# Kernel optimization log

Hardware: AMD Instinct MI355X
Metric: run time of the kernel (lower is better)

## Reference

```python
import jax, jax.numpy as jnp
import numpy as np

H = 1024
B = 8
T = 2048

def setup_inputs() -> dict:
    key = jax.random.key(0)
    ks = jax.random.split(key, 12)
    s = 1.0 / np.sqrt(H)
    return {
        "x": jax.random.normal(ks[0], (B, T, H), dtype=jnp.float32),
        "time_decay": jax.random.normal(ks[1], (H,), dtype=jnp.float32) * 0.1,
        "time_first": jax.random.normal(ks[2], (H,), dtype=jnp.float32) * 0.1,
        "time_mix_key": jax.random.uniform(ks[3], (1, 1, H), dtype=jnp.float32),
        "time_mix_value": jax.random.uniform(ks[4], (1, 1, H), dtype=jnp.float32),
        "time_mix_receptance": jax.random.uniform(ks[5], (1, 1, H), dtype=jnp.float32),
        "Wk": jax.random.normal(ks[6], (H, H), dtype=jnp.float32) * s,
        "Wv": jax.random.normal(ks[7], (H, H), dtype=jnp.float32) * s,
        "Wr": jax.random.normal(ks[8], (H, H), dtype=jnp.float32) * s,
        "Wo": jax.random.normal(ks[9], (H, H), dtype=jnp.float32) * s,
        "bo": jax.random.normal(ks[10], (H,), dtype=jnp.float32) * 0.01,
    }

def reference(x, time_decay, time_first, time_mix_key, time_mix_value,
              time_mix_receptance, Wk, Wv, Wr, Wo, bo):
    # time shift: shifted[:, t] = x[:, t-1], shifted[:, 0] = 0
    shifted = jnp.pad(x, ((0, 0), (1, 0), (0, 0)))[:, :-1]
    k_in = x * time_mix_key + shifted * (1.0 - time_mix_key)
    v_in = x * time_mix_value + shifted * (1.0 - time_mix_value)
    r_in = x * time_mix_receptance + shifted * (1.0 - time_mix_receptance)
    k = jnp.einsum('bth,oh->bto', k_in, Wk)
    v = jnp.einsum('bth,oh->bto', v_in, Wv)
    r = jax.nn.sigmoid(jnp.einsum('bth,oh->bto', r_in, Wr))

    td = jnp.exp(-jnp.exp(time_decay))  # (H,)

    def step(carry, kv):
        num, den = carry            # (B, H) each
        k_t, v_t = kv               # (B, H) each
        e = jnp.exp(time_first + k_t)
        out_t = (num + e * v_t) / (den + e)
        ek = jnp.exp(k_t)
        return (td * num + ek * v_t, td * den + ek), out_t

    init = (jnp.zeros((x.shape[0], x.shape[2]), x.dtype),
            jnp.zeros((x.shape[0], x.shape[2]), x.dtype))
    # scan over time: (T, B, H)
    _, wkv = jax.lax.scan(step, init, (k.transpose(1, 0, 2), v.transpose(1, 0, 2)))
    wkv = wkv.transpose(1, 0, 2)    # (B, T, H)

    return jnp.einsum('bth,oh->bto', r * wkv, Wo) + bo
```

## Files before the change

kernel.cpp:

```cpp
#include <hip/hip_runtime.h>
#include <hip/hip_bf16.h>
#include <cstdint>
#include <cstddef>

#define HH 1024
#define BB 8
#define TT 2048
#define MM (BB*TT)
#define CC 128
#define LL (TT/CC)

typedef __attribute__((ext_vector_type(8))) short bf16x8;
typedef __attribute__((ext_vector_type(8))) unsigned short u16x8;
typedef __attribute__((ext_vector_type(4))) float f32x4;

__device__ __forceinline__ unsigned short f2bf(float f) {
  union { float f; unsigned u; } v; v.f = f;
  return (unsigned short)((v.u + 0x7fffu + ((v.u >> 16) & 1u)) >> 16);
}
__device__ __forceinline__ float bf2f(unsigned short s) {
  union { float f; unsigned u; } v; v.u = ((unsigned)s) << 16;
  return v.f;
}

__device__ __forceinline__ void load_lds16(const void* g, void* l) {
  __builtin_amdgcn_global_load_lds((const __attribute__((address_space(1))) void*)g,
                                   (__attribute__((address_space(3))) void*)l,
                                   16, 0, 0);
}

__global__ __launch_bounds__(256) void conv_w(const float* __restrict__ Wk,
    const float* __restrict__ Wv, const float* __restrict__ Wr,
    const float* __restrict__ Wo, unsigned short* __restrict__ dst) {
  const int i = (blockIdx.x * 256 + threadIdx.x) * 4;
  const float* src = blockIdx.y == 0 ? Wk : blockIdx.y == 1 ? Wv : blockIdx.y == 2 ? Wr : Wo;
  const float4 v = *(const float4*)(src + i);
  ushort4 o; o.x = f2bf(v.x); o.y = f2bf(v.y); o.z = f2bf(v.z); o.w = f2bf(v.w);
  *(ushort4*)(dst + (size_t)blockIdx.y * HH * HH + i) = o;
}

__global__ __launch_bounds__(256) void mix_kernel(const float* __restrict__ x,
    const float* __restrict__ tmk, const float* __restrict__ tmv, const float* __restrict__ tmr,
    unsigned short* __restrict__ kin, unsigned short* __restrict__ vin,
    unsigned short* __restrict__ rin) {
  const int gid = blockIdx.x * 256 + threadIdx.x;
  const size_t e0 = (size_t)gid * 4;
  const int h = (int)(e0 & (HH - 1));
  const int t = (int)((e0 >> 10) & (TT - 1));
  const float4 xv = *(const float4*)(x + e0);
  float4 sv = make_float4(0.f, 0.f, 0.f, 0.f);
  if (t != 0) sv = *(const float4*)(x + e0 - HH);
  const float4 k4 = *(const float4*)(tmk + h);
  const float4 v4 = *(const float4*)(tmv + h);
  const float4 r4 = *(const float4*)(tmr + h);
  ushort4 ko, vo, ro;
  ko.x = f2bf(sv.x + k4.x * (xv.x - sv.x)); ko.y = f2bf(sv.y + k4.y * (xv.y - sv.y));
  ko.z = f2bf(sv.z + k4.z * (xv.z - sv.z)); ko.w = f2bf(sv.w + k4.w * (xv.w - sv.w));
  vo.x = f2bf(sv.x + v4.x * (xv.x - sv.x)); vo.y = f2bf(sv.y + v4.y * (xv.y - sv.y));
  vo.z = f2bf(sv.z + v4.z * (xv.z - sv.z)); vo.w = f2bf(sv.w + v4.w * (xv.w - sv.w));
  ro.x = f2bf(sv.x + r4.x * (xv.x - sv.x)); ro.y = f2bf(sv.y + r4.y * (xv.y - sv.y));
  ro.z = f2bf(sv.z + r4.z * (xv.z - sv.z)); ro.w = f2bf(sv.w + r4.w * (xv.w - sv.w));
  *(ushort4*)(kin + e0) = ko;
  *(ushort4*)(vin + e0) = vo;
  *(ushort4*)(rin + e0) = ro;
}


#define BAR()   do { asm volatile("" ::: "memory"); __builtin_amdgcn_s_barrier(); \
                     asm volatile("" ::: "memory"); } while (0)
#define LGKM0() asm volatile("s_waitcnt lgkmcnt(0)" ::: "memory")
#define VM6()   asm volatile("s_waitcnt vmcnt(6)" ::: "memory")
#define VM0()   asm volatile("s_waitcnt vmcnt(0)" ::: "memory")

__device__ __forceinline__ void stA(const unsigned short* __restrict__ Ag, int m0, int kt,
                                    unsigned short* buf, int h, int w, int rl, int scol) {
#pragma unroll
  for (int l = 0; l < 2; ++l) {
    const int row = l * 128 + h * 64 + w * 8;
    load_lds16(Ag + (size_t)(m0 + row + rl) * HH + kt + scol, buf + row * 64);
  }
}
__device__ __forceinline__ void stB(const unsigned short* __restrict__ Bg, int n0, int kt,
                                    unsigned short* buf, int h, int w, int rl, int scol) {
#pragma unroll
  for (int l = 0; l < 2; ++l) {
    const int row = (2 * (l * 2 + (w >> 2)) + h) * 32 + (w & 3) * 8;
    load_lds16(Bg + (size_t)(n0 + row + rl) * HH + kt + scol, buf + row * 64);
  }
}

template<int MH>
__device__ __forceinline__ void rdA(const unsigned short* buf, bf16x8 (&af)[4][2],
                                    int wm, int l15, int kq, int swz) {
#pragma unroll
  for (int fm = 0; fm < 4; ++fm)
#pragma unroll
    for (int kk = 0; kk < 2; ++kk)
      af[fm][kk] = *(const bf16x8*)(buf + (wm * 128 + MH * 64 + fm * 16 + l15) * 64
                                        + ((kk * 32 + kq * 8) ^ swz));
}
template<int NH>
__device__ __forceinline__ void rdB(const unsigned short* buf, bf16x8 (&bfr)[2][2][2],
                                    int wn, int l15, int kq, int swz) {
#pragma unroll
  for (int fn = 0; fn < 2; ++fn)
#pragma unroll
    for (int kk = 0; kk < 2; ++kk)
      bfr[NH][fn][kk] = *(const bf16x8*)(buf + (wn * 64 + NH * 32 + fn * 16 + l15) * 64
                                             + ((kk * 32 + kq * 8) ^ swz));
}
template<int MH, int NH>
__device__ __forceinline__ void mfmaQ(f32x4 (&acc)[8][4], const bf16x8 (&af)[4][2],
                                      const bf16x8 (&bfr)[2][2][2]) {
  __builtin_amdgcn_s_setprio(1);
#pragma unroll
  for (int kk = 0; kk < 2; ++kk)
#pragma unroll
    for (int fm = 0; fm < 4; ++fm)
#pragma unroll
      for (int fn = 0; fn < 2; ++fn)
        acc[MH * 4 + fm][NH * 2 + fn] = __builtin_amdgcn_mfma_f32_16x16x32_bf16(
            af[fm][kk], bfr[NH][fn][kk], acc[MH * 4 + fm][NH * 2 + fn], 0, 0, 0);
  __builtin_amdgcn_s_setprio(0);
}

__device__ __forceinline__ void gemm256(const unsigned short* __restrict__ Ag,
                                        const unsigned short* __restrict__ Bg,
                                        const int m0, const int n0,
                                        unsigned short* As, unsigned short* Bs,
                                        f32x4 (&acc)[8][4]) {
  const int tid = threadIdx.x;
  const int lane = tid & 63;
  const int w = tid >> 6;
  const int wm = w >> 2, wn = w & 3;
  const int l15 = lane & 15, kq = lane >> 4;
  const int swz = (l15 & 7) << 3;
  const int rl = lane >> 3;
  const int scol = ((lane & 7) ^ rl) * 8;
  unsigned short* const A0 = As;
  unsigned short* const A1 = As + 256 * 64;
  unsigned short* const B0 = Bs;
  unsigned short* const B1 = Bs + 256 * 64;
  bf16x8 af[4][2], bfr[2][2][2];

  stA(Ag, m0, 0, A0, 0, w, rl, scol);
  stB(Bg, n0, 0, B0, 0, w, rl, scol);
  stB(Bg, n0, 0, B0, 1, w, rl, scol);
  stA(Ag, m0, 0, A0, 1, w, rl, scol);
  stA(Ag, m0, 64, A1, 0, w, rl, scol);
  stB(Bg, n0, 64, B1, 0, w, rl, scol);
  stB(Bg, n0, 64, B1, 1, w, rl, scol);
  VM6(); BAR();

#pragma unroll 1
  for (int i = 0; i < 8; ++i) {
    const int tb1 = ((2 * i + 1) * 64) & (HH - 1);
    const int tn0 = ((2 * i + 2) * 64) & (HH - 1);
    const int tn1 = ((2 * i + 3) * 64) & (HH - 1);
    rdA<0>(A0, af, wm, l15, kq, swz); rdB<0>(B0, bfr, wn, l15, kq, swz);
    stA(Ag, m0, tb1, A1, 1, w, rl, scol);
    BAR(); LGKM0(); mfmaQ<0, 0>(acc, af, bfr); BAR();
    rdB<1>(B0, bfr, wn, l15, kq, swz);
    stA(Ag, m0, tn0, A0, 0, w, rl, scol);
    BAR(); LGKM0(); mfmaQ<0, 1>(acc, af, bfr); BAR();
    rdA<1>(A0, af, wm, l15, kq, swz);
    stB(Bg, n0, tn0, B0, 0, w, rl, scol);
    BAR(); LGKM0(); mfmaQ<1, 1>(acc, af, bfr); BAR();
    stB(Bg, n0, tn0, B0, 1, w, rl, scol);
    VM6(); BAR(); LGKM0(); mfmaQ<1, 0>(acc, af, bfr); BAR();
    rdA<0>(A1, af, wm, l15, kq, swz); rdB<0>(B1, bfr, wn, l15, kq, swz);
    stA(Ag, m0, tn0, A0, 1, w, rl, scol);
    BAR(); LGKM0(); mfmaQ<0, 0>(acc, af, bfr); BAR();
    rdB<1>(B1, bfr, wn, l15, kq, swz);
    stA(Ag, m0, tn1, A1, 0, w, rl, scol);
    BAR(); LGKM0(); mfmaQ<0, 1>(acc, af, bfr); BAR();
    rdA<1>(A1, af, wm, l15, kq, swz);
    stB(Bg, n0, tn1, B1, 0, w, rl, scol);
    BAR(); LGKM0(); mfmaQ<1, 1>(acc, af, bfr); BAR();
    stB(Bg, n0, tn1, B1, 1, w, rl, scol);
    VM6(); BAR(); LGKM0(); mfmaQ<1, 0>(acc, af, bfr); BAR();
  }
  VM0();
}

__device__ __forceinline__ void swizzle_mn256(int x, int& m0, int& n0) {
  const int wg = (x & 7) * 32 + (x >> 3);
  m0 = (wg >> 2) * 256;
  n0 = (wg & 3) * 256;
}

__global__ __launch_bounds__(512, 2) void gemm_kvr(const unsigned short* __restrict__ kin,
    const unsigned short* __restrict__ vin, const unsigned short* __restrict__ rin,
    const unsigned short* __restrict__ Wbf,
    unsigned short* __restrict__ kb, unsigned short* __restrict__ vb,
    unsigned short* __restrict__ rb) {
  __shared__ unsigned short As[2 * 256 * 64];
  __shared__ unsigned short Bs[2 * 256 * 64];
  const int z = blockIdx.y;
  const unsigned short* Ag = z == 0 ? kin : (z == 1 ? vin : rin);
  const unsigned short* Bg = Wbf + (size_t)z * HH * HH;
  unsigned short* Cg = z == 0 ? kb : (z == 1 ? vb : rb);
  int m0, n0; swizzle_mn256(blockIdx.x, m0, n0);
  f32x4 acc[8][4] = {};
  gemm256(Ag, Bg, m0, n0, As, Bs, acc);
  const int lane = threadIdx.x & 63, w = threadIdx.x >> 6;
  const int wm = w >> 2, wn = w & 3, l15 = lane & 15, lq = lane >> 4;
  const bool sig = (z == 2);
#pragma unroll
  for (int fm = 0; fm < 8; ++fm)
#pragma unroll
    for (int fn = 0; fn < 4; ++fn) {
      const int col = n0 + wn * 64 + fn * 16 + l15;
      const int r0 = m0 + wm * 128 + fm * 16 + lq * 4;
#pragma unroll
      for (int j = 0; j < 4; ++j) {
        float vv = acc[fm][fn][j];
        if (sig) vv = 1.0f / (1.0f + __expf(-vv));
        Cg[(size_t)(r0 + j) * HH + col] = f2bf(vv);
      }
    }
}

__global__ __launch_bounds__(512, 2) void gemm_o(const unsigned short* __restrict__ Ag,
    const unsigned short* __restrict__ Bg, const float* __restrict__ bias,
    float* __restrict__ C) {
  __shared__ unsigned short As[2 * 256 * 64];
  __shared__ unsigned short Bs[2 * 256 * 64];
  int m0, n0; swizzle_mn256(blockIdx.x, m0, n0);
  f32x4 acc[8][4] = {};
  gemm256(Ag, Bg, m0, n0, As, Bs, acc);
  const int lane = threadIdx.x & 63, w = threadIdx.x >> 6;
  const int wm = w >> 2, wn = w & 3, l15 = lane & 15, lq = lane >> 4;
#pragma unroll
  for (int fm = 0; fm < 8; ++fm)
#pragma unroll
    for (int fn = 0; fn < 4; ++fn) {
      const int col = n0 + wn * 64 + fn * 16 + l15;
      const float bv = bias[col];
      const int r0 = m0 + wm * 128 + fm * 16 + lq * 4;
#pragma unroll
      for (int j = 0; j < 4; ++j)
        C[(size_t)(r0 + j) * HH + col] = acc[fm][fn][j] + bv;
    }
}

__global__ __launch_bounds__(256) void wkv_part(const unsigned short* __restrict__ k,
    const unsigned short* __restrict__ v, const float* __restrict__ tdec,
    float* __restrict__ pnum, float* __restrict__ pden) {
  const int gid = blockIdx.x * 256 + threadIdx.x;
  const int h0 = (gid & 127) * 8;
  const int b = (gid >> 7) & (BB - 1);
  const int c = gid >> 10;
  float td[8], num[8], den[8];
#pragma unroll
  for (int j = 0; j < 8; ++j) {
    td[j] = __expf(-__expf(tdec[h0 + j]));
    num[j] = 0.f; den[j] = 0.f;
  }
  size_t idx = (size_t)b * TT * HH + (size_t)(c * LL) * HH + h0;
#pragma unroll 4
  for (int i = 0; i < LL; ++i, idx += HH) {
    const u16x8 k8 = *(const u16x8*)(k + idx);
    const u16x8 v8 = *(const u16x8*)(v + idx);
#pragma unroll
    for (int j = 0; j < 8; ++j) {
      const float ek = __expf(bf2f(k8[j]));
      num[j] = td[j] * num[j] + ek * bf2f(v8[j]);
      den[j] = td[j] * den[j] + ek;
    }
  }
  const size_t o = (size_t)c * (BB * HH) + b * HH + h0;
#pragma unroll
  for (int j = 0; j < 8; ++j) { pnum[o + j] = num[j]; pden[o + j] = den[j]; }
}

__global__ __launch_bounds__(256) void wkv_scan(const float* __restrict__ tdec,
    float* __restrict__ pnum, float* __restrict__ pden) {
  const int bh = blockIdx.x * 256 + threadIdx.x;
  const int h = bh & (HH - 1);
  const float ed = __expf(tdec[h]);
  const float tdL = __expf(-ed * (float)LL);
  float num = 0.f, den = 0.f;
#pragma unroll 8
  for (int c = 0; c < CC; ++c) {
    const size_t o = (size_t)c * (BB * HH) + bh;
    const float tn = pnum[o], td_ = pden[o];
    pnum[o] = num; pden[o] = den;
    num = tdL * num + tn;
    den = tdL * den + td_;
  }
}

__global__ __launch_bounds__(256) void wkv_final(const unsigned short* __restrict__ k,
    const unsigned short* __restrict__ v, const unsigned short* __restrict__ r,
    const float* __restrict__ tdec, const float* __restrict__ tfst,
    const float* __restrict__ pnum, const float* __restrict__ pden,
    unsigned short* __restrict__ rwkv) {
  const int gid = blockIdx.x * 256 + threadIdx.x;
  const int h0 = (gid & 127) * 8;
  const int b = (gid >> 7) & (BB - 1);
  const int c = gid >> 10;
  float td[8], etf[8], num[8], den[8];
  const size_t o = (size_t)c * (BB * HH) + b * HH + h0;
#pragma unroll
  for (int j = 0; j < 8; ++j) {
    td[j] = __expf(-__expf(tdec[h0 + j]));
    etf[j] = __expf(tfst[h0 + j]);
    num[j] = pnum[o + j]; den[j] = pden[o + j];
  }
  size_t idx = (size_t)b * TT * HH + (size_t)(c * LL) * HH + h0;
#pragma unroll 2
  for (int i = 0; i < LL; ++i, idx += HH) {
    const u16x8 k8 = *(const u16x8*)(k + idx);
    const u16x8 v8 = *(const u16x8*)(v + idx);
    const u16x8 r8 = *(const u16x8*)(r + idx);
    u16x8 o8;
#pragma unroll
    for (int j = 0; j < 8; ++j) {
      const float ek = __expf(bf2f(k8[j]));
      const float vt = bf2f(v8[j]);
      const float rt = bf2f(r8[j]);
      const float e = ek * etf[j];
      const float inv = __builtin_amdgcn_rcpf(den[j] + e);
      const float outv = (num[j] + e * vt) * inv;
      num[j] = td[j] * num[j] + ek * vt;
      den[j] = td[j] * den[j] + ek;
      o8[j] = f2bf(outv * rt);
    }
    *(u16x8*)(rwkv + idx) = o8;
  }
}

extern "C" void kernel_launch(void* const* d_in, const int* in_sizes, int n_in,
                              void* d_out, int out_size, void* d_ws, size_t ws_size,
                              hipStream_t stream) {
  (void)in_sizes; (void)n_in; (void)out_size; (void)ws_size;
  const float* x    = (const float*)d_in[0];
  const float* tdec = (const float*)d_in[1];
  const float* tfst = (const float*)d_in[2];
  const float* tmk  = (const float*)d_in[3];
  const float* tmv  = (const float*)d_in[4];
  const float* tmr  = (const float*)d_in[5];
  const float* Wk   = (const float*)d_in[6];
  const float* Wv   = (const float*)d_in[7];
  const float* Wr   = (const float*)d_in[8];
  const float* Wo   = (const float*)d_in[9];
  const float* bo   = (const float*)d_in[10];
  float* out = (float*)d_out;

  char* ws = (char*)d_ws;
  const size_t MiB = (size_t)1 << 20;
  unsigned short* Wbf = (unsigned short*)(ws);
  unsigned short* kin = (unsigned short*)(ws + 8 * MiB);
  unsigned short* vin = (unsigned short*)(ws + 40 * MiB);
  unsigned short* rin = (unsigned short*)(ws + 72 * MiB);
  unsigned short* rb  = (unsigned short*)(ws + 104 * MiB);
  unsigned short* kb = (unsigned short*)out;
  unsigned short* vb = kb + (size_t)MM * HH;
  unsigned short* rwkv = kin;
  float* pnum = (float*)(ws + 40 * MiB);
  float* pden = (float*)(ws + 44 * MiB);

  hipLaunchKernelGGL(conv_w, dim3(1024, 4), dim3(256), 0, stream, Wk, Wv, Wr, Wo, Wbf);
  hipLaunchKernelGGL(mix_kernel, dim3(16384), dim3(256), 0, stream,
                     x, tmk, tmv, tmr, kin, vin, rin);
  hipLaunchKernelGGL(gemm_kvr, dim3(256, 3), dim3(512), 0, stream,
                     kin, vin, rin, Wbf, kb, vb, rb);
  hipLaunchKernelGGL(wkv_part, dim3(512), dim3(256), 0, stream,
                     kb, vb, tdec, pnum, pden);
  hipLaunchKernelGGL(wkv_scan, dim3(32), dim3(256), 0, stream,
                     tdec, pnum, pden);
  hipLaunchKernelGGL(wkv_final, dim3(512), dim3(256), 0, stream,
                     kb, vb, rb, tdec, tfst, pnum, pden, rwkv);
  hipLaunchKernelGGL(gemm_o, dim3(256), dim3(512), 0, stream,
                     rwkv, Wbf + (size_t)3 * HH * HH, bo, out);
}
```

Measured before the change: 348.0 us.

## Reschedule GEMM main loop, transpose MFMA outputs for vector stores, double scan chunks

Restructures the bf16 GEMM inner loop: LDS fragment reads are split into halves with sched_barriers, the MFMA operands are swapped so each lane holds four consecutive columns, and the prefetch order changes so the loop waits at vmcnt(4) instead of vmcnt(6). Epilogues in both GEMMs now write ushort4/float4 vector stores instead of scalar strided stores. The WKV chunk count doubles to 256 with fully unrolled shorter chunks and twice the grid, and the pden buffer offset moves to fit. The intent is to overlap LDS reads, global prefetch and MFMAs better, coalesce output writes, and expose more parallelism in the scan, at the cost of more partial-state traffic and register pressure.

```diff
diff --git a/kernel.cpp b/kernel.cpp
--- a/kernel.cpp
+++ b/kernel.cpp
@@ -7,7 +7,7 @@
 #define BB 8
 #define TT 2048
 #define MM (BB*TT)
-#define CC 128
+#define CC 256
 #define LL (TT/CC)
 
 typedef __attribute__((ext_vector_type(8))) short bf16x8;
@@ -68,8 +68,8 @@
 
 #define BAR()   do { asm volatile("" ::: "memory"); __builtin_amdgcn_s_barrier(); \
                      asm volatile("" ::: "memory"); } while (0)
-#define LGKM0() asm volatile("s_waitcnt lgkmcnt(0)" ::: "memory")
-#define VM6()   asm volatile("s_waitcnt vmcnt(6)" ::: "memory")
+#define SB0()   __builtin_amdgcn_sched_barrier(0)
+#define VM4()   asm volatile("s_waitcnt vmcnt(4)" ::: "memory")
 #define VM0()   asm volatile("s_waitcnt vmcnt(0)" ::: "memory")
 
 __device__ __forceinline__ void stA(const unsigned short* __restrict__ Ag, int m0, int kt,
@@ -89,11 +89,11 @@
   }
 }
 
-template<int MH>
-__device__ __forceinline__ void rdA(const unsigned short* buf, bf16x8 (&af)[4][2],
-                                    int wm, int l15, int kq, int swz) {
-#pragma unroll
-  for (int fm = 0; fm < 4; ++fm)
+template<int MH, int FH>
+__device__ __forceinline__ void rdA_h(const unsigned short* buf, bf16x8 (&af)[4][2],
+                                      int wm, int l15, int kq, int swz) {
+#pragma unroll
+  for (int fm = FH * 2; fm < FH * 2 + 2; ++fm)
 #pragma unroll
     for (int kk = 0; kk < 2; ++kk)
       af[fm][kk] = *(const bf16x8*)(buf + (wm * 128 + MH * 64 + fm * 16 + l15) * 64
@@ -109,19 +109,17 @@
       bfr[NH][fn][kk] = *(const bf16x8*)(buf + (wn * 64 + NH * 32 + fn * 16 + l15) * 64
                                              + ((kk * 32 + kq * 8) ^ swz));
 }
-template<int MH, int NH>
-__device__ __forceinline__ void mfmaQ(f32x4 (&acc)[8][4], const bf16x8 (&af)[4][2],
+template<int MH, int NH, int FH>
+__device__ __forceinline__ void mfma8(f32x4 (&acc)[8][4], const bf16x8 (&af)[4][2],
                                       const bf16x8 (&bfr)[2][2][2]) {
-  __builtin_amdgcn_s_setprio(1);
 #pragma unroll
   for (int kk = 0; kk < 2; ++kk)
 #pragma unroll
-    for (int fm = 0; fm < 4; ++fm)
+    for (int fm = FH * 2; fm < FH * 2 + 2; ++fm)
 #pragma unroll
       for (int fn = 0; fn < 2; ++fn)
         acc[MH * 4 + fm][NH * 2 + fn] = __builtin_amdgcn_mfma_f32_16x16x32_bf16(
-            af[fm][kk], bfr[NH][fn][kk], acc[MH * 4 + fm][NH * 2 + fn], 0, 0, 0);
-  __builtin_amdgcn_s_setprio(0);
+            bfr[NH][fn][kk], af[fm][kk], acc[MH * 4 + fm][NH * 2 + fn], 0, 0, 0);
 }
 
 __device__ __forceinline__ void gemm256(const unsigned short* __restrict__ Ag,
@@ -149,36 +147,69 @@
   stA(Ag, m0, 0, A0, 1, w, rl, scol);
   stA(Ag, m0, 64, A1, 0, w, rl, scol);
   stB(Bg, n0, 64, B1, 0, w, rl, scol);
-  stB(Bg, n0, 64, B1, 1, w, rl, scol);
-  VM6(); BAR();
+  VM4();
+  BAR();
 
 #pragma unroll 1
   for (int i = 0; i < 8; ++i) {
-    const int tb1 = ((2 * i + 1) * 64) & (HH - 1);
+    const int t1  = ((2 * i + 1) * 64) & (HH - 1);
     const int tn0 = ((2 * i + 2) * 64) & (HH - 1);
     const int tn1 = ((2 * i + 3) * 64) & (HH - 1);
-    rdA<0>(A0, af, wm, l15, kq, swz); rdB<0>(B0, bfr, wn, l15, kq, swz);
-    stA(Ag, m0, tb1, A1, 1, w, rl, scol);
-    BAR(); LGKM0(); mfmaQ<0, 0>(acc, af, bfr); BAR();
+
+    rdA_h<0, 0>(A0, af, wm, l15, kq, swz); SB0();
+    rdB<0>(B0, bfr, wn, l15, kq, swz);     SB0();
+    rdA_h<0, 1>(A0, af, wm, l15, kq, swz); SB0();
     rdB<1>(B0, bfr, wn, l15, kq, swz);
+    stB(Bg, n0, t1, B1, 1, w, rl, scol);
+    stA(Ag, m0, t1, A1, 1, w, rl, scol);
+    BAR(); SB0();
+    __builtin_amdgcn_s_setprio(1);
+    mfma8<0, 0, 0>(acc, af, bfr); SB0();
+    mfma8<0, 0, 1>(acc, af, bfr); SB0();
+    mfma8<0, 1, 0>(acc, af, bfr);
+    mfma8<0, 1, 1>(acc, af, bfr);
+    __builtin_amdgcn_s_setprio(0);
+    BAR();
+    rdA_h<1, 0>(A0, af, wm, l15, kq, swz); SB0();
+    rdA_h<1, 1>(A0, af, wm, l15, kq, swz);
     stA(Ag, m0, tn0, A0, 0, w, rl, scol);
-    BAR(); LGKM0(); mfmaQ<0, 1>(acc, af, bfr); BAR();
-    rdA<1>(A0, af, wm, l15, kq, swz);
     stB(Bg, n0, tn0, B0, 0, w, rl, scol);
-    BAR(); LGKM0(); mfmaQ<1, 1>(acc, af, bfr); BAR();
+    BAR(); SB0();
+    __builtin_amdgcn_s_setprio(1);
+    mfma8<1, 0, 0>(acc, af, bfr);
+    mfma8<1, 1, 0>(acc, af, bfr); SB0();
+    mfma8<1, 0, 1>(acc, af, bfr);
+    mfma8<1, 1, 1>(acc, af, bfr);
+    __builtin_amdgcn_s_setprio(0);
+    VM4();
+    BAR();
+    rdA_h<0, 0>(A1, af, wm, l15, kq, swz); SB0();
+    rdB<0>(B1, bfr, wn, l15, kq, swz);     SB0();
+    rdA_h<0, 1>(A1, af, wm, l15, kq, swz); SB0();
+    rdB<1>(B1, bfr, wn, l15, kq, swz);
     stB(Bg, n0, tn0, B0, 1, w, rl, scol);
-    VM6(); BAR(); LGKM0(); mfmaQ<1, 0>(acc, af, bfr); BAR();
-    rdA<0>(A1, af, wm, l15, kq, swz); rdB<0>(B1, bfr, wn, l15, kq, swz);
     stA(Ag, m0, tn0, A0, 1, w, rl, scol);
-    BAR(); LGKM0(); mfmaQ<0, 0>(acc, af, bfr); BAR();
-    rdB<1>(B1, bfr, wn, l15, kq, swz);
+    BAR(); SB0();
+    __builtin_amdgcn_s_setprio(1);
+    mfma8<0, 0, 0>(acc, af, bfr); SB0();
+    mfma8<0, 0, 1>(acc, af, bfr); SB0();
+    mfma8<0, 1, 0>(acc, af, bfr);
+    mfma8<0, 1, 1>(acc, af, bfr);
+    __builtin_amdgcn_s_setprio(0);
+    BAR();
+    rdA_h<1, 0>(A1, af, wm, l15, kq, swz); SB0();
+    rdA_h<1, 1>(A1, af, wm, l15, kq, swz);
     stA(Ag, m0, tn1, A1, 0, w, rl, scol);
-    BAR(); LGKM0(); mfmaQ<0, 1>(acc, af, bfr); BAR();
-    rdA<1>(A1, af, wm, l15, kq, swz);
     stB(Bg, n0, tn1, B1, 0, w, rl, scol);
-    BAR(); LGKM0(); mfmaQ<1, 1>(acc, af, bfr); BAR();
-    stB(Bg, n0, tn1, B1, 1, w, rl, scol);
-    VM6(); BAR(); LGKM0(); mfmaQ<1, 0>(acc, af, bfr); BAR();
+    BAR(); SB0();
+    __builtin_amdgcn_s_setprio(1);
+    mfma8<1, 0, 0>(acc, af, bfr);
+    mfma8<1, 1, 0>(acc, af, bfr); SB0();
+    mfma8<1, 0, 1>(acc, af, bfr);
+    mfma8<1, 1, 1>(acc, af, bfr);
+    __builtin_amdgcn_s_setprio(0);
+    VM4();
+    BAR();
   }
   VM0();
 }
@@ -207,18 +238,21 @@
   const int wm = w >> 2, wn = w & 3, l15 = lane & 15, lq = lane >> 4;
   const bool sig = (z == 2);
 #pragma unroll
-  for (int fm = 0; fm < 8; ++fm)
+  for (int fm = 0; fm < 8; ++fm) {
+    const size_t mrow = (size_t)(m0 + wm * 128 + fm * 16 + l15) * HH;
 #pragma unroll
     for (int fn = 0; fn < 4; ++fn) {
-      const int col = n0 + wn * 64 + fn * 16 + l15;
-      const int r0 = m0 + wm * 128 + fm * 16 + lq * 4;
-#pragma unroll
-      for (int j = 0; j < 4; ++j) {
-        float vv = acc[fm][fn][j];
-        if (sig) vv = 1.0f / (1.0f + __expf(-vv));
-        Cg[(size_t)(r0 + j) * HH + col] = f2bf(vv);
+      const int ncol = n0 + wn * 64 + fn * 16 + lq * 4;
+      float v0 = acc[fm][fn][0], v1 = acc[fm][fn][1];
+      float v2 = acc[fm][fn][2], v3 = acc[fm][fn][3];
+      if (sig) {
+        v0 = 1.0f / (1.0f + __expf(-v0)); v1 = 1.0f / (1.0f + __expf(-v1));
+        v2 = 1.0f / (1.0f + __expf(-v2)); v3 = 1.0f / (1.0f + __expf(-v3));
       }
+      ushort4 o; o.x = f2bf(v0); o.y = f2bf(v1); o.z = f2bf(v2); o.w = f2bf(v3);
+      *(ushort4*)(Cg + mrow + ncol) = o;
     }
+  }
 }
 
 __global__ __launch_bounds__(512, 2) void gemm_o(const unsigned short* __restrict__ Ag,
@@ -232,16 +266,18 @@
   const int lane = threadIdx.x & 63, w = threadIdx.x >> 6;
   const int wm = w >> 2, wn = w & 3, l15 = lane & 15, lq = lane >> 4;
 #pragma unroll
-  for (int fm = 0; fm < 8; ++fm)
+  for (int fm = 0; fm < 8; ++fm) {
+    const size_t mrow = (size_t)(m0 + wm * 128 + fm * 16 + l15) * HH;
 #pragma unroll
     for (int fn = 0; fn < 4; ++fn) {
-      const int col = n0 + wn * 64 + fn * 16 + l15;
-      const float bv = bias[col];
-      const int r0 = m0 + wm * 128 + fm * 16 + lq * 4;
-#pragma unroll
-      for (int j = 0; j < 4; ++j)
-        C[(size_t)(r0 + j) * HH + col] = acc[fm][fn][j] + bv;
+      const int ncol = n0 + wn * 64 + fn * 16 + lq * 4;
+      const float4 bv = *(const float4*)(bias + ncol);
+      float4 ov;
+      ov.x = acc[fm][fn][0] + bv.x; ov.y = acc[fm][fn][1] + bv.y;
+      ov.z = acc[fm][fn][2] + bv.z; ov.w = acc[fm][fn][3] + bv.w;
+      *(float4*)(C + mrow + ncol) = ov;
     }
+  }
 }
 
 __global__ __launch_bounds__(256) void wkv_part(const unsigned short* __restrict__ k,
@@ -258,7 +294,7 @@
     num[j] = 0.f; den[j] = 0.f;
   }
   size_t idx = (size_t)b * TT * HH + (size_t)(c * LL) * HH + h0;
-#pragma unroll 4
+#pragma unroll
   for (int i = 0; i < LL; ++i, idx += HH) {
     const u16x8 k8 = *(const u16x8*)(k + idx);
     const u16x8 v8 = *(const u16x8*)(v + idx);
@@ -309,7 +345,7 @@
     num[j] = pnum[o + j]; den[j] = pden[o + j];
   }
   size_t idx = (size_t)b * TT * HH + (size_t)(c * LL) * HH + h0;
-#pragma unroll 2
+#pragma unroll
   for (int i = 0; i < LL; ++i, idx += HH) {
     const u16x8 k8 = *(const u16x8*)(k + idx);
     const u16x8 v8 = *(const u16x8*)(v + idx);
@@ -359,18 +395,18 @@
   unsigned short* vb = kb + (size_t)MM * HH;
   unsigned short* rwkv = kin;
   float* pnum = (float*)(ws + 40 * MiB);
-  float* pden = (float*)(ws + 44 * MiB);
+  float* pden = (float*)(ws + 48 * MiB);
 
   hipLaunchKernelGGL(conv_w, dim3(1024, 4), dim3(256), 0, stream, Wk, Wv, Wr, Wo, Wbf);
   hipLaunchKernelGGL(mix_kernel, dim3(16384), dim3(256), 0, stream,
                      x, tmk, tmv, tmr, kin, vin, rin);
   hipLaunchKernelGGL(gemm_kvr, dim3(256, 3), dim3(512), 0, stream,
                      kin, vin, rin, Wbf, kb, vb, rb);
-  hipLaunchKernelGGL(wkv_part, dim3(512), dim3(256), 0, stream,
+  hipLaunchKernelGGL(wkv_part, dim3(1024), dim3(256), 0, stream,
                      kb, vb, tdec, pnum, pden);
   hipLaunchKernelGGL(wkv_scan, dim3(32), dim3(256), 0, stream,
                      tdec, pnum, pden);
-  hipLaunchKernelGGL(wkv_final, dim3(512), dim3(256), 0, stream,
+  hipLaunchKernelGGL(wkv_final, dim3(1024), dim3(256), 0, stream,
                      kb, vb, rb, tdec, tfst, pnum, pden, rwkv);
   hipLaunchKernelGGL(gemm_o, dim3(256), dim3(512), 0, stream,
                      rwkv, Wbf + (size_t)3 * HH * HH, bo, out);
```

Result: slower. 374.1 us (+7.5%).

## Fuse prep kernels, swap MFMA operands for vectorized epilogue stores, adjust waits

Applied to the files above, without the earlier changes.

Merges the weight conversion and token-mix kernels into one launch to save a kernel launch. Swaps the A/B operands of the MFMA so each lane holds four consecutive columns, which lets the GEMM epilogues write ushort4/float4 vectors instead of scattered scalar stores. Drops the explicit lgkmcnt(0) waits and leaves LDS wait insertion to the compiler, moves setprio to wrap each MFMA group, and reorders the LDS reads.

```diff
diff --git a/kernel.cpp b/kernel.cpp
--- a/kernel.cpp
+++ b/kernel.cpp
@@ -29,48 +29,52 @@
                                    16, 0, 0);
 }
 
-__global__ __launch_bounds__(256) void conv_w(const float* __restrict__ Wk,
-    const float* __restrict__ Wv, const float* __restrict__ Wr,
-    const float* __restrict__ Wo, unsigned short* __restrict__ dst) {
-  const int i = (blockIdx.x * 256 + threadIdx.x) * 4;
-  const float* src = blockIdx.y == 0 ? Wk : blockIdx.y == 1 ? Wv : blockIdx.y == 2 ? Wr : Wo;
-  const float4 v = *(const float4*)(src + i);
-  ushort4 o; o.x = f2bf(v.x); o.y = f2bf(v.y); o.z = f2bf(v.z); o.w = f2bf(v.w);
-  *(ushort4*)(dst + (size_t)blockIdx.y * HH * HH + i) = o;
-}
-
-__global__ __launch_bounds__(256) void mix_kernel(const float* __restrict__ x,
+__global__ __launch_bounds__(256) void prep(const float* __restrict__ x,
     const float* __restrict__ tmk, const float* __restrict__ tmv, const float* __restrict__ tmr,
+    const float* __restrict__ Wk, const float* __restrict__ Wv,
+    const float* __restrict__ Wr, const float* __restrict__ Wo,
     unsigned short* __restrict__ kin, unsigned short* __restrict__ vin,
-    unsigned short* __restrict__ rin) {
-  const int gid = blockIdx.x * 256 + threadIdx.x;
-  const size_t e0 = (size_t)gid * 4;
-  const int h = (int)(e0 & (HH - 1));
-  const int t = (int)((e0 >> 10) & (TT - 1));
-  const float4 xv = *(const float4*)(x + e0);
-  float4 sv = make_float4(0.f, 0.f, 0.f, 0.f);
-  if (t != 0) sv = *(const float4*)(x + e0 - HH);
-  const float4 k4 = *(const float4*)(tmk + h);
-  const float4 v4 = *(const float4*)(tmv + h);
-  const float4 r4 = *(const float4*)(tmr + h);
-  ushort4 ko, vo, ro;
-  ko.x = f2bf(sv.x + k4.x * (xv.x - sv.x)); ko.y = f2bf(sv.y + k4.y * (xv.y - sv.y));
-  ko.z = f2bf(sv.z + k4.z * (xv.z - sv.z)); ko.w = f2bf(sv.w + k4.w * (xv.w - sv.w));
-  vo.x = f2bf(sv.x + v4.x * (xv.x - sv.x)); vo.y = f2bf(sv.y + v4.y * (xv.y - sv.y));
-  vo.z = f2bf(sv.z + v4.z * (xv.z - sv.z)); vo.w = f2bf(sv.w + v4.w * (xv.w - sv.w));
-  ro.x = f2bf(sv.x + r4.x * (xv.x - sv.x)); ro.y = f2bf(sv.y + r4.y * (xv.y - sv.y));
-  ro.z = f2bf(sv.z + r4.z * (xv.z - sv.z)); ro.w = f2bf(sv.w + r4.w * (xv.w - sv.w));
-  *(ushort4*)(kin + e0) = ko;
-  *(ushort4*)(vin + e0) = vo;
-  *(ushort4*)(rin + e0) = ro;
+    unsigned short* __restrict__ rin, unsigned short* __restrict__ Wbf) {
+  const int bx = blockIdx.x;
+  if (bx < 16384) {
+    const int gid = bx * 256 + threadIdx.x;
+    const size_t e0 = (size_t)gid * 4;
+    const int h = (int)(e0 & (HH - 1));
+    const int t = (int)((e0 >> 10) & (TT - 1));
+    const float4 xv = *(const float4*)(x + e0);
+    float4 sv = make_float4(0.f, 0.f, 0.f, 0.f);
+    if (t != 0) sv = *(const float4*)(x + e0 - HH);
+    const float4 k4 = *(const float4*)(tmk + h);
+    const float4 v4 = *(const float4*)(tmv + h);
+    const float4 r4 = *(const float4*)(tmr + h);
+    ushort4 ko, vo, ro;
+    ko.x = f2bf(sv.x + k4.x * (xv.x - sv.x)); ko.y = f2bf(sv.y + k4.y * (xv.y - sv.y));
+    ko.z = f2bf(sv.z + k4.z * (xv.z - sv.z)); ko.w = f2bf(sv.w + k4.w * (xv.w - sv.w));
+    vo.x = f2bf(sv.x + v4.x * (xv.x - sv.x)); vo.y = f2bf(sv.y + v4.y * (xv.y - sv.y));
+    vo.z = f2bf(sv.z + v4.z * (xv.z - sv.z)); vo.w = f2bf(sv.w + v4.w * (xv.w - sv.w));
+    ro.x = f2bf(sv.x + r4.x * (xv.x - sv.x)); ro.y = f2bf(sv.y + r4.y * (xv.y - sv.y));
+    ro.z = f2bf(sv.z + r4.z * (xv.z - sv.z)); ro.w = f2bf(sv.w + r4.w * (xv.w - sv.w));
+    *(ushort4*)(kin + e0) = ko;
+    *(ushort4*)(vin + e0) = vo;
+    *(ushort4*)(rin + e0) = ro;
+  } else {
+    const int q = bx - 16384;
+    const int zz = q >> 10;
+    const float* src = zz == 0 ? Wk : zz == 1 ? Wv : zz == 2 ? Wr : Wo;
+    const int i = ((q & 1023) * 256 + threadIdx.x) * 4;
+    const float4 v = *(const float4*)(src + i);
+    ushort4 o; o.x = f2bf(v.x); o.y = f2bf(v.y); o.z = f2bf(v.z); o.w = f2bf(v.w);
+    *(ushort4*)(Wbf + (size_t)zz * HH * HH + i) = o;
+  }
 }
 
 
 #define BAR()   do { asm volatile("" ::: "memory"); __builtin_amdgcn_s_barrier(); \
                      asm volatile("" ::: "memory"); } while (0)
-#define LGKM0() asm volatile("s_waitcnt lgkmcnt(0)" ::: "memory")
 #define VM6()   asm volatile("s_waitcnt vmcnt(6)" ::: "memory")
 #define VM0()   asm volatile("s_waitcnt vmcnt(0)" ::: "memory")
+#define PRIO1() __builtin_amdgcn_s_setprio(1)
+#define PRIO0() __builtin_amdgcn_s_setprio(0)
 
 __device__ __forceinline__ void stA(const unsigned short* __restrict__ Ag, int m0, int kt,
                                     unsigned short* buf, int h, int w, int rl, int scol) {
@@ -93,9 +97,9 @@
 __device__ __forceinline__ void rdA(const unsigned short* buf, bf16x8 (&af)[4][2],
                                     int wm, int l15, int kq, int swz) {
 #pragma unroll
-  for (int fm = 0; fm < 4; ++fm)
-#pragma unroll
-    for (int kk = 0; kk < 2; ++kk)
+  for (int kk = 0; kk < 2; ++kk)
+#pragma unroll
+    for (int fm = 0; fm < 4; ++fm)
       af[fm][kk] = *(const bf16x8*)(buf + (wm * 128 + MH * 64 + fm * 16 + l15) * 64
                                         + ((kk * 32 + kq * 8) ^ swz));
 }
@@ -103,16 +107,15 @@
 __device__ __forceinline__ void rdB(const unsigned short* buf, bf16x8 (&bfr)[2][2][2],
                                     int wn, int l15, int kq, int swz) {
 #pragma unroll
-  for (int fn = 0; fn < 2; ++fn)
-#pragma unroll
-    for (int kk = 0; kk < 2; ++kk)
+  for (int kk = 0; kk < 2; ++kk)
+#pragma unroll
+    for (int fn = 0; fn < 2; ++fn)
       bfr[NH][fn][kk] = *(const bf16x8*)(buf + (wn * 64 + NH * 32 + fn * 16 + l15) * 64
                                              + ((kk * 32 + kq * 8) ^ swz));
 }
 template<int MH, int NH>
 __device__ __forceinline__ void mfmaQ(f32x4 (&acc)[8][4], const bf16x8 (&af)[4][2],
                                       const bf16x8 (&bfr)[2][2][2]) {
-  __builtin_amdgcn_s_setprio(1);
 #pragma unroll
   for (int kk = 0; kk < 2; ++kk)
 #pragma unroll
@@ -120,8 +123,7 @@
 #pragma unroll
       for (int fn = 0; fn < 2; ++fn)
         acc[MH * 4 + fm][NH * 2 + fn] = __builtin_amdgcn_mfma_f32_16x16x32_bf16(
-            af[fm][kk], bfr[NH][fn][kk], acc[MH * 4 + fm][NH * 2 + fn], 0, 0, 0);
-  __builtin_amdgcn_s_setprio(0);
+            bfr[NH][fn][kk], af[fm][kk], acc[MH * 4 + fm][NH * 2 + fn], 0, 0, 0);
 }
 
 __device__ __forceinline__ void gemm256(const unsigned short* __restrict__ Ag,
@@ -157,28 +159,30 @@
     const int tb1 = ((2 * i + 1) * 64) & (HH - 1);
     const int tn0 = ((2 * i + 2) * 64) & (HH - 1);
     const int tn1 = ((2 * i + 3) * 64) & (HH - 1);
-    rdA<0>(A0, af, wm, l15, kq, swz); rdB<0>(B0, bfr, wn, l15, kq, swz);
+    rdB<0>(B0, bfr, wn, l15, kq, swz);
+    rdA<0>(A0, af, wm, l15, kq, swz);
     stA(Ag, m0, tb1, A1, 1, w, rl, scol);
-    BAR(); LGKM0(); mfmaQ<0, 0>(acc, af, bfr); BAR();
+    BAR(); PRIO1(); mfmaQ<0, 0>(acc, af, bfr); PRIO0(); BAR();
     rdB<1>(B0, bfr, wn, l15, kq, swz);
     stA(Ag, m0, tn0, A0, 0, w, rl, scol);
-    BAR(); LGKM0(); mfmaQ<0, 1>(acc, af, bfr); BAR();
+    BAR(); PRIO1(); mfmaQ<0, 1>(acc, af, bfr); PRIO0(); BAR();
     rdA<1>(A0, af, wm, l15, kq, swz);
     stB(Bg, n0, tn0, B0, 0, w, rl, scol);
-    BAR(); LGKM0(); mfmaQ<1, 1>(acc, af, bfr); BAR();
+    BAR(); PRIO1(); mfmaQ<1, 1>(acc, af, bfr); PRIO0(); BAR();
     stB(Bg, n0, tn0, B0, 1, w, rl, scol);
-    VM6(); BAR(); LGKM0(); mfmaQ<1, 0>(acc, af, bfr); BAR();
-    rdA<0>(A1, af, wm, l15, kq, swz); rdB<0>(B1, bfr, wn, l15, kq, swz);
+    VM6(); BAR(); PRIO1(); mfmaQ<1, 0>(acc, af, bfr); PRIO0(); BAR();
+    rdB<0>(B1, bfr, wn, l15, kq, swz);
+    rdA<0>(A1, af, wm, l15, kq, swz);
     stA(Ag, m0, tn0, A0, 1, w, rl, scol);
-    BAR(); LGKM0(); mfmaQ<0, 0>(acc, af, bfr); BAR();
+    BAR(); PRIO1(); mfmaQ<0, 0>(acc, af, bfr); PRIO0(); BAR();
     rdB<1>(B1, bfr, wn, l15, kq, swz);
     stA(Ag, m0, tn1, A1, 0, w, rl, scol);
-    BAR(); LGKM0(); mfmaQ<0, 1>(acc, af, bfr); BAR();
+    BAR(); PRIO1(); mfmaQ<0, 1>(acc, af, bfr); PRIO0(); BAR();
     rdA<1>(A1, af, wm, l15, kq, swz);
     stB(Bg, n0, tn1, B1, 0, w, rl, scol);
-    BAR(); LGKM0(); mfmaQ<1, 1>(acc, af, bfr); BAR();
+    BAR(); PRIO1(); mfmaQ<1, 1>(acc, af, bfr); PRIO0(); BAR();
     stB(Bg, n0, tn1, B1, 1, w, rl, scol);
-    VM6(); BAR(); LGKM0(); mfmaQ<1, 0>(acc, af, bfr); BAR();
+    VM6(); BAR(); PRIO1(); mfmaQ<1, 0>(acc, af, bfr); PRIO0(); BAR();
   }
   VM0();
 }
@@ -207,18 +211,21 @@
   const int wm = w >> 2, wn = w & 3, l15 = lane & 15, lq = lane >> 4;
   const bool sig = (z == 2);
 #pragma unroll
-  for (int fm = 0; fm < 8; ++fm)
+  for (int fm = 0; fm < 8; ++fm) {
+    const size_t mrow = (size_t)(m0 + wm * 128 + fm * 16 + l15) * HH;
 #pragma unroll
     for (int fn = 0; fn < 4; ++fn) {
-      const int col = n0 + wn * 64 + fn * 16 + l15;
-      const int r0 = m0 + wm * 128 + fm * 16 + lq * 4;
-#pragma unroll
-      for (int j = 0; j < 4; ++j) {
-        float vv = acc[fm][fn][j];
-        if (sig) vv = 1.0f / (1.0f + __expf(-vv));
-        Cg[(size_t)(r0 + j) * HH + col] = f2bf(vv);
+      const int ncol = n0 + wn * 64 + fn * 16 + lq * 4;
+      float v0 = acc[fm][fn][0], v1 = acc[fm][fn][1];
+      float v2 = acc[fm][fn][2], v3 = acc[fm][fn][3];
+      if (sig) {
+        v0 = 1.0f / (1.0f + __expf(-v0)); v1 = 1.0f / (1.0f + __expf(-v1));
+        v2 = 1.0f / (1.0f + __expf(-v2)); v3 = 1.0f / (1.0f + __expf(-v3));
       }
+      ushort4 o; o.x = f2bf(v0); o.y = f2bf(v1); o.z = f2bf(v2); o.w = f2bf(v3);
+      *(ushort4*)(Cg + mrow + ncol) = o;
     }
+  }
 }
 
 __global__ __launch_bounds__(512, 2) void gemm_o(const unsigned short* __restrict__ Ag,
@@ -232,16 +239,18 @@
   const int lane = threadIdx.x & 63, w = threadIdx.x >> 6;
   const int wm = w >> 2, wn = w & 3, l15 = lane & 15, lq = lane >> 4;
 #pragma unroll
-  for (int fm = 0; fm < 8; ++fm)
+  for (int fm = 0; fm < 8; ++fm) {
+    const size_t mrow = (size_t)(m0 + wm * 128 + fm * 16 + l15) * HH;
 #pragma unroll
     for (int fn = 0; fn < 4; ++fn) {
-      const int col = n0 + wn * 64 + fn * 16 + l15;
-      const float bv = bias[col];
-      const int r0 = m0 + wm * 128 + fm * 16 + lq * 4;
-#pragma unroll
-      for (int j = 0; j < 4; ++j)
-        C[(size_t)(r0 + j) * HH + col] = acc[fm][fn][j] + bv;
+      const int ncol = n0 + wn * 64 + fn * 16 + lq * 4;
+      const float4 bv = *(const float4*)(bias + ncol);
+      float4 ov;
+      ov.x = acc[fm][fn][0] + bv.x; ov.y = acc[fm][fn][1] + bv.y;
+      ov.z = acc[fm][fn][2] + bv.z; ov.w = acc[fm][fn][3] + bv.w;
+      *(float4*)(C + mrow + ncol) = ov;
     }
+  }
 }
 
 __global__ __launch_bounds__(256) void wkv_part(const unsigned short* __restrict__ k,
@@ -361,9 +370,8 @@
   float* pnum = (float*)(ws + 40 * MiB);
   float* pden = (float*)(ws + 44 * MiB);
 
-  hipLaunchKernelGGL(conv_w, dim3(1024, 4), dim3(256), 0, stream, Wk, Wv, Wr, Wo, Wbf);
-  hipLaunchKernelGGL(mix_kernel, dim3(16384), dim3(256), 0, stream,
-                     x, tmk, tmv, tmr, kin, vin, rin);
+  hipLaunchKernelGGL(prep, dim3(20480), dim3(256), 0, stream,
+                     x, tmk, tmv, tmr, Wk, Wv, Wr, Wo, kin, vin, rin, Wbf);
   hipLaunchKernelGGL(gemm_kvr, dim3(256, 3), dim3(512), 0, stream,
                      kin, vin, rin, Wbf, kb, vb, rb);
   hipLaunchKernelGGL(wkv_part, dim3(512), dim3(256), 0, stream,
```

Result: slower. 360.8 us (+3.7%).
